# Optimization experiments

Measured on AMD Instinct MI355X. Metric: run time of the kernel, lower is better.

The kernel has to match this reference:

```python
import jax, jax.numpy as jnp
import numpy as np

B, T, V, E, H, FC, O = 4096, 64, 512, 32, 128, 256, 1024


def setup_inputs() -> dict:
    key = jax.random.key(0)
    ks = jax.random.split(key, 12)
    n = lambda k, shape, sc=1.0: (jax.random.normal(k, shape, jnp.float32) * sc)
    return {
        "message": n(ks[0], (B, T, V), 0.1),
        "W_emb": n(ks[1], (E, V), 0.05),
        "b_emb": n(ks[2], (E,), 0.05),
        "init_emb": n(ks[3], (1, 1, E), 1.0),
        "W_ih": n(ks[4], (3 * H, E), 0.08),
        "W_hh": n(ks[5], (3 * H, H), 0.08),
        "b_ih": n(ks[6], (3 * H,), 0.05),
        "b_hh": n(ks[7], (3 * H,), 0.05),
        "W_fc1": n(ks[8], (FC, H), 0.08),
        "b_fc1": n(ks[9], (FC,), 0.05),
        "W_fc2": n(ks[10], (O, FC), 0.05),
        "b_fc2": n(ks[11], (O,), 0.05),
    }


def reference(message, W_emb, b_emb, init_emb, W_ih, W_hh, b_ih, b_hh,
              W_fc1, b_fc1, W_fc2, b_fc2):
    Bb, Tt, Vv = message.shape
    Hh = W_hh.shape[1]
    # Per-step embedding of the message (torch does this inside the loop;
    # it is a pure per-timestep linear so we batch it once): [B,T,E]
    emb = jnp.einsum('btv,ev->bte', message, W_emb) + b_emb
    # Inputs consumed by the GRU at step t: initial_embedding at t=0,
    # then embedding(message[:, t-1]) for t >= 1. The embedding of the
    # final token is computed in torch but never fed to the GRU.
    x0 = jnp.broadcast_to(init_emb[0], (Bb, init_emb.shape[-1]))  # [B,E]
    xs = jnp.concatenate([x0[:, None, :], emb[:, :Tt - 1, :]], axis=1)  # [B,T,E]
    # Precompute input-side gate pre-activations for all steps: [T,B,3H]
    gi_all = jnp.einsum('bte,ge->tbg', xs, W_ih) + b_ih

    def gru_step(h, gi):
        gh = h @ W_hh.T + b_hh  # [B,3H]
        i_r, i_z, i_n = jnp.split(gi, 3, axis=-1)
        h_r, h_z, h_n = jnp.split(gh, 3, axis=-1)
        r = jax.nn.sigmoid(i_r + h_r)
        z = jax.nn.sigmoid(i_z + h_z)
        nng = jnp.tanh(i_n + r * h_n)
        h_new = (1.0 - z) * nng + z * h
        return h_new, None

    h0 = jnp.zeros((Bb, Hh), message.dtype)
    h_last, _ = jax.lax.scan(gru_step, h0, gi_all)
    hid = jax.nn.elu(h_last @ W_fc1.T + b_fc1)
    return jax.nn.sigmoid(hid @ W_fc2.T + b_fc2)
```

## Files before the change

### kernel.cpp

```cpp
#include <hip/hip_runtime.h>
#include <math.h>

#define B_ 4096
#define T_ 64
#define V_ 512
#define E_ 32
#define H_ 128
#define FC1_ 256
#define O_ 1024

typedef float f32x4 __attribute__((ext_vector_type(4)));
typedef short s16x8 __attribute__((ext_vector_type(8)));
typedef unsigned short u16;

#define MFMA16(a, b, c) __builtin_amdgcn_mfma_f32_16x16x32_bf16(a, b, c, 0, 0, 0)

union Frag { u16 q[8]; unsigned u[4]; s16x8 v; };

__device__ __forceinline__ u16 f2bf(float f) {
    union { float f; unsigned u; } v; v.f = f;
    unsigned r = v.u + 0x7FFFu + ((v.u >> 16) & 1u);
    return (u16)(r >> 16);
}
__device__ __forceinline__ unsigned cvtpk(float lo, float hi) {
    unsigned r;
    asm("v_cvt_pk_bf16_f32 %0, %1, %2" : "=v"(r) : "v"(lo), "v"(hi));
    return r;
}
__device__ __forceinline__ float sigf(float x) { return 1.0f / (1.0f + __expf(-x)); }
__device__ __forceinline__ float tanhfast(float x) {
    return 1.0f - 2.0f / (__expf(2.0f * x) + 1.0f);
}
__device__ __forceinline__ void gll16(const float* gsrc, float* ldst) {
    __builtin_amdgcn_global_load_lds(
        (const __attribute__((address_space(1))) unsigned int*)gsrc,
        (__attribute__((address_space(3))) unsigned int*)ldst,
        16, 0, 0);
}
__device__ __forceinline__ s16x8 gatherB(const float* W, int row, int K, int k0, int lh) {
    const float* p = W + (size_t)row * K + k0 + lh * 8;
    float4 a = *(const float4*)p;
    float4 b = *(const float4*)(p + 4);
    Frag f;
    f.u[0] = cvtpk(a.x, a.y); f.u[1] = cvtpk(a.z, a.w);
    f.u[2] = cvtpk(b.x, b.y); f.u[3] = cvtpk(b.z, b.w);
    return f.v;
}

__global__ void __launch_bounds__(512, 2) fused_kernel(
    const float* __restrict__ msg,
    const float* __restrict__ Wemb, const float* __restrict__ b_emb,
    const float* __restrict__ init_emb,
    const float* __restrict__ Wih, const float* __restrict__ Whh,
    const float* __restrict__ b_ih, const float* __restrict__ b_hh,
    const float* __restrict__ Wfc1, const float* __restrict__ b_fc1,
    const float* __restrict__ Wfc2, const float* __restrict__ b_fc2,
    float* __restrict__ out) {
    __shared__ float mlds[2][16][516];
    __shared__ u16 hlds[2][16 * 136];
    __shared__ float epart[2][8][576];
    __shared__ u16 xfrag[2][640];
    __shared__ u16 hidl[16 * 264];
    const int tid = threadIdx.x, w = tid >> 6, l = tid & 63;
    const int ln = l & 15, lh = l >> 4;
    const int wg = w & 3, wp = w >> 2;
    const int gb = blockIdx.x;

    for (int i = tid; i < 16 * 136; i += 512) hlds[0][i] = 0;

#define GLL_COL(C, BUF) do {                                                   \
    _Pragma("unroll")                                                          \
    for (int i_ = 0; i_ < 4; i_++) {                                           \
        int r_ = 2 * w + (i_ >> 1);                                            \
        int h_ = (i_ & 1) * 256;                                               \
        gll16(msg + ((size_t)(gb * 16 + r_) * T_ + (C)) * V_ + h_ + l * 4,     \
              &mlds[BUF][r_][h_]);                                             \
    }                                                                          \
} while (0)

    GLL_COL(0, 0);
    GLL_COL(1, 1);

    s16x8 wh[3][4], wi[3], we[2][2];
    float br, bz, bin, bgn;
    {
        #pragma unroll
        for (int g = 0; g < 3; g++) {
            int gt = wg + 4 * wp + 8 * g;
            #pragma unroll
            for (int kc = 0; kc < 4; kc++)
                wh[g][kc] = gatherB(Whh, gt * 16 + ln, 128, kc * 32, lh);
            wi[g] = gatherB(Wih, gt * 16 + ln, 32, 0, lh);
        }
        #pragma unroll
        for (int kk = 0; kk < 2; kk++) {
            we[kk][0] = gatherB(Wemb, ln, 512, (2 * w + kk) * 32, lh);
            we[kk][1] = gatherB(Wemb, 16 + ln, 512, (2 * w + kk) * 32, lh);
        }
        int c = wg * 16 + wp * 64 + ln;
        br  = b_ih[c] + b_hh[c];
        bz  = b_ih[128 + c] + b_hh[128 + c];
        bin = b_ih[256 + c];
        bgn = b_hh[256 + c];
    }
    const float bev = b_emb[tid & 31];
    s16x8 xinit;
    {
        Frag xi;
        #pragma unroll
        for (int j = 0; j < 8; j++) xi.q[j] = f2bf(init_emb[lh * 8 + j]);
        xinit = xi.v;
    }
    float hold[4] = {};
    __syncthreads();

#define EMBED_LDS(BUF, PAR) do {                                               \
    f32x4 e0 = {0.f, 0.f, 0.f, 0.f}, e1 = {0.f, 0.f, 0.f, 0.f};                \
    _Pragma("unroll")                                                          \
    for (int kk = 0; kk < 2; kk++) {                                           \
        const float* mp = &mlds[BUF][ln][(2 * w + kk) * 32 + lh * 8];          \
        f32x4 m0 = *(const f32x4*)mp;                                          \
        f32x4 m1 = *(const f32x4*)(mp + 4);                                    \
        Frag fa;                                                               \
        fa.u[0] = cvtpk(m0[0], m0[1]); fa.u[1] = cvtpk(m0[2], m0[3]);          \
        fa.u[2] = cvtpk(m1[0], m1[1]); fa.u[3] = cvtpk(m1[2], m1[3]);          \
        e0 = MFMA16(fa.v, we[kk][0], e0);                                      \
        e1 = MFMA16(fa.v, we[kk][1], e1);                                      \
    }                                                                          \
    _Pragma("unroll")                                                          \
    for (int i = 0; i < 4; i++) {                                              \
        epart[PAR][w][(lh * 4 + i) * 36 + ln]      = e0[i];                    \
        epart[PAR][w][(lh * 4 + i) * 36 + 16 + ln] = e1[i];                    \
    }                                                                          \
} while (0)

    EMBED_LDS(0, 1);
    __syncthreads();

    const int aoff = ln * 136 + lh * 8;
    const int colo = wg * 16 + wp * 64 + ln;
    const int fr = tid >> 5, fc = tid & 31, fo = fr * 36 + fc;

#define GRU_STEP(TT) do {                                                      \
    const int t = (TT);                                                        \
    if (t <= 60) GLL_COL(t + 2, t & 1);                                        \
    const u16* hb = hlds[t & 1];                                               \
    s16x8 af0 = *(const s16x8*)(hb + aoff);                                    \
    s16x8 af1 = *(const s16x8*)(hb + aoff + 32);                               \
    s16x8 af2 = *(const s16x8*)(hb + aoff + 64);                               \
    s16x8 af3 = *(const s16x8*)(hb + aoff + 96);                               \
    s16x8 xc;                                                                  \
    if (t == 0) xc = xinit;                                                    \
    else xc = *(const s16x8*)(&xfrag[(t + 1) & 1][0] + ln * 40 + lh * 8);      \
    f32x4 ar  = {br, br, br, br};                                              \
    f32x4 az  = {bz, bz, bz, bz};                                              \
    f32x4 agn = {bgn, bgn, bgn, bgn};                                          \
    f32x4 ain = {bin, bin, bin, bin};                                          \
    ar  = MFMA16(xc, wi[0], ar);                                               \
    az  = MFMA16(xc, wi[1], az);                                               \
    ain = MFMA16(xc, wi[2], ain);                                              \
    ar  = MFMA16(af0, wh[0][0], ar);                                           \
    ar  = MFMA16(af1, wh[0][1], ar);                                           \
    ar  = MFMA16(af2, wh[0][2], ar);                                           \
    ar  = MFMA16(af3, wh[0][3], ar);                                           \
    az  = MFMA16(af0, wh[1][0], az);                                           \
    az  = MFMA16(af1, wh[1][1], az);                                           \
    az  = MFMA16(af2, wh[1][2], az);                                           \
    az  = MFMA16(af3, wh[1][3], az);                                           \
    agn = MFMA16(af0, wh[2][0], agn);                                          \
    agn = MFMA16(af1, wh[2][1], agn);                                          \
    agn = MFMA16(af2, wh[2][2], agn);                                          \
    agn = MFMA16(af3, wh[2][3], agn);                                          \
    u16* hw = hlds[(t + 1) & 1];                                               \
    float hn[4];                                                               \
    _Pragma("unroll")                                                          \
    for (int i = 0; i < 4; i++) {                                              \
        float rg = sigf(ar[i]);                                                \
        float zg = sigf(az[i]);                                                \
        float ng = tanhfast(ain[i] + rg * agn[i]);                             \
        hn[i] = zg * (hold[i] - ng) + ng;                                      \
        hold[i] = hn[i];                                                       \
    }                                                                          \
    {                                                                          \
        unsigned u01 = cvtpk(hn[0], hn[1]);                                    \
        unsigned u23 = cvtpk(hn[2], hn[3]);                                    \
        hw[(lh * 4 + 0) * 136 + colo] = (u16)(u01 & 0xFFFFu);                  \
        hw[(lh * 4 + 1) * 136 + colo] = (u16)(u01 >> 16);                      \
        hw[(lh * 4 + 2) * 136 + colo] = (u16)(u23 & 0xFFFFu);                  \
        hw[(lh * 4 + 3) * 136 + colo] = (u16)(u23 >> 16);                      \
    }                                                                          \
    if (t <= 61) EMBED_LDS((t + 1) & 1, t & 1);                                \
    if (t <= 62) {                                                             \
        const float* eb = &epart[(t + 1) & 1][0][0];                           \
        float s = eb[fo]           + eb[576 + fo]     + eb[2 * 576 + fo]       \
                + eb[3 * 576 + fo] + eb[4 * 576 + fo] + eb[5 * 576 + fo]       \
                + eb[6 * 576 + fo] + eb[7 * 576 + fo] + bev;                   \
        xfrag[t & 1][fr * 40 + fc] = f2bf(s);                                  \
    }                                                                          \
    __syncthreads();                                                           \
} while (0)

    for (int tt = 0; tt < 64; tt += 2) {
        GRU_STEP(tt);
        GRU_STEP(tt + 1);
    }
#undef GRU_STEP
#undef GLL_COL
#undef EMBED_LDS

    const u16* hb = hlds[0];
    s16x8 hf0 = *(const s16x8*)(hb + aoff);
    s16x8 hf1 = *(const s16x8*)(hb + aoff + 32);
    s16x8 hf2 = *(const s16x8*)(hb + aoff + 64);
    s16x8 hf3 = *(const s16x8*)(hb + aoff + 96);
    #pragma unroll
    for (int q = 0; q < 2; q++) {
        int ot = 2 * w + q;
        float b1 = b_fc1[ot * 16 + ln];
        f32x4 a1 = {b1, b1, b1, b1};
        a1 = MFMA16(hf0, gatherB(Wfc1, ot * 16 + ln, 128, 0,  lh), a1);
        a1 = MFMA16(hf1, gatherB(Wfc1, ot * 16 + ln, 128, 32, lh), a1);
        a1 = MFMA16(hf2, gatherB(Wfc1, ot * 16 + ln, 128, 64, lh), a1);
        a1 = MFMA16(hf3, gatherB(Wfc1, ot * 16 + ln, 128, 96, lh), a1);
        #pragma unroll
        for (int i = 0; i < 4; i++) {
            float v = a1[i];
            v = v > 0.0f ? v : (__expf(v) - 1.0f);
            hidl[(lh * 4 + i) * 264 + ot * 16 + ln] = f2bf(v);
        }
    }
    __syncthreads();

    s16x8 hf[8];
    #pragma unroll
    for (int kc = 0; kc < 8; kc++)
        hf[kc] = *(const s16x8*)(hidl + ln * 264 + kc * 32 + lh * 8);
    #pragma unroll
    for (int q = 0; q < 8; q++) {
        int nt = 8 * w + q;
        float b2 = b_fc2[nt * 16 + ln];
        f32x4 a2 = {b2, b2, b2, b2};
        #pragma unroll
        for (int kc = 0; kc < 8; kc++)
            a2 = MFMA16(hf[kc], gatherB(Wfc2, nt * 16 + ln, 256, kc * 32, lh), a2);
        #pragma unroll
        for (int i = 0; i < 4; i++)
            out[(size_t)(gb * 16 + lh * 4 + i) * 1024 + nt * 16 + ln] = sigf(a2[i]);
    }
}

extern "C" void kernel_launch(void* const* d_in, const int* in_sizes, int n_in,
                              void* d_out, int out_size, void* d_ws, size_t ws_size,
                              hipStream_t stream) {
    const float* message  = (const float*)d_in[0];
    const float* W_emb    = (const float*)d_in[1];
    const float* b_emb    = (const float*)d_in[2];
    const float* init_emb = (const float*)d_in[3];
    const float* W_ih     = (const float*)d_in[4];
    const float* W_hh     = (const float*)d_in[5];
    const float* b_ih     = (const float*)d_in[6];
    const float* b_hh     = (const float*)d_in[7];
    const float* W_fc1    = (const float*)d_in[8];
    const float* b_fc1    = (const float*)d_in[9];
    const float* W_fc2    = (const float*)d_in[10];
    const float* b_fc2    = (const float*)d_in[11];
    float* out = (float*)d_out;
    (void)d_ws; (void)ws_size;

    hipLaunchKernelGGL(fused_kernel, dim3(256), dim3(512), 0, stream,
                       message, W_emb, b_emb, init_emb, W_ih, W_hh, b_ih, b_hh,
                       W_fc1, b_fc1, W_fc2, b_fc2, out);
}
```

Baseline: 158.1 us.

## Triple-buffer message prefetch with partial vmcnt barriers in GRU loop

Moves the message-column prefetch to three LDS buffers so loads are issued three steps ahead, and replaces __syncthreads with an explicit barrier that waits only until at most 4 global loads remain outstanding. This lets each wave keep one step's async global-to-LDS copies in flight across the barrier instead of draining them every step. The initial embedding is now written into xfrag up front so the t==0 branch disappears, and the loop is unrolled by 6 with compile-time buffer indices. The hidl buffer is aliased onto epart to offset the added LDS, which could still affect occupancy, and the hand-tuned vmcnt count must match the loads actually issued.

```diff
diff --git a/kernel.cpp b/kernel.cpp
--- a/kernel.cpp
+++ b/kernel.cpp
@@ -46,6 +46,16 @@
     f.u[2] = cvtpk(b.x, b.y); f.u[3] = cvtpk(b.z, b.w);
     return f.v;
 }
+
+#define STEP_BARRIER() do {                                        \
+    asm volatile("s_waitcnt vmcnt(4) lgkmcnt(0)" ::: "memory");    \
+    __builtin_amdgcn_s_barrier();                                  \
+    __builtin_amdgcn_sched_barrier(0);                             \
+} while (0)
+#define LDS_BARRIER() do {                                         \
+    asm volatile("s_waitcnt lgkmcnt(0)" ::: "memory");             \
+    __builtin_amdgcn_s_barrier();                                  \
+} while (0)
 
 __global__ void __launch_bounds__(512, 2) fused_kernel(
     const float* __restrict__ msg,
@@ -56,17 +66,21 @@
     const float* __restrict__ Wfc1, const float* __restrict__ b_fc1,
     const float* __restrict__ Wfc2, const float* __restrict__ b_fc2,
     float* __restrict__ out) {
-    __shared__ float mlds[2][16][516];
+    __shared__ float mlds[3][16][516];
     __shared__ u16 hlds[2][16 * 136];
     __shared__ float epart[2][8][576];
     __shared__ u16 xfrag[2][640];
-    __shared__ u16 hidl[16 * 264];
+    u16* const hidl = (u16*)&epart[0][0][0];
     const int tid = threadIdx.x, w = tid >> 6, l = tid & 63;
     const int ln = l & 15, lh = l >> 4;
     const int wg = w & 3, wp = w >> 2;
     const int gb = blockIdx.x;
 
     for (int i = tid; i < 16 * 136; i += 512) hlds[0][i] = 0;
+    {
+        int fr = tid >> 5, fc = tid & 31;
+        xfrag[1][fr * 40 + fc] = f2bf(init_emb[fc]);
+    }
 
 #define GLL_COL(C, BUF) do {                                                   \
     _Pragma("unroll")                                                          \
@@ -80,6 +94,7 @@
 
     GLL_COL(0, 0);
     GLL_COL(1, 1);
+    GLL_COL(2, 2);
 
     s16x8 wh[3][4], wi[3], we[2][2];
     float br, bz, bin, bgn;
@@ -104,13 +119,6 @@
         bgn = b_hh[256 + c];
     }
     const float bev = b_emb[tid & 31];
-    s16x8 xinit;
-    {
-        Frag xi;
-        #pragma unroll
-        for (int j = 0; j < 8; j++) xi.q[j] = f2bf(init_emb[lh * 8 + j]);
-        xinit = xi.v;
-    }
     float hold[4] = {};
     __syncthreads();
 
@@ -135,23 +143,21 @@
 } while (0)
 
     EMBED_LDS(0, 1);
-    __syncthreads();
+    LDS_BARRIER();
 
     const int aoff = ln * 136 + lh * 8;
     const int colo = wg * 16 + wp * 64 + ln;
     const int fr = tid >> 5, fc = tid & 31, fo = fr * 36 + fc;
 
-#define GRU_STEP(TT) do {                                                      \
+#define GRU_STEP(TT, K, ISSUE, EMB, RED) do {                                  \
     const int t = (TT);                                                        \
-    if (t <= 60) GLL_COL(t + 2, t & 1);                                        \
-    const u16* hb = hlds[t & 1];                                               \
+    if (ISSUE) GLL_COL(t + 3, (K) % 3);                                        \
+    const u16* hb = hlds[(K) & 1];                                             \
     s16x8 af0 = *(const s16x8*)(hb + aoff);                                    \
     s16x8 af1 = *(const s16x8*)(hb + aoff + 32);                               \
     s16x8 af2 = *(const s16x8*)(hb + aoff + 64);                               \
     s16x8 af3 = *(const s16x8*)(hb + aoff + 96);                               \
-    s16x8 xc;                                                                  \
-    if (t == 0) xc = xinit;                                                    \
-    else xc = *(const s16x8*)(&xfrag[(t + 1) & 1][0] + ln * 40 + lh * 8);      \
+    s16x8 xc = *(const s16x8*)(&xfrag[((K) + 1) & 1][0] + ln * 40 + lh * 8);   \
     f32x4 ar  = {br, br, br, br};                                              \
     f32x4 az  = {bz, bz, bz, bz};                                              \
     f32x4 agn = {bgn, bgn, bgn, bgn};                                          \
@@ -171,7 +177,7 @@
     agn = MFMA16(af1, wh[2][1], agn);                                          \
     agn = MFMA16(af2, wh[2][2], agn);                                          \
     agn = MFMA16(af3, wh[2][3], agn);                                          \
-    u16* hw = hlds[(t + 1) & 1];                                               \
+    u16* hw = hlds[((K) + 1) & 1];                                             \
     float hn[4];                                                               \
     _Pragma("unroll")                                                          \
     for (int i = 0; i < 4; i++) {                                              \
@@ -189,21 +195,29 @@
         hw[(lh * 4 + 2) * 136 + colo] = (u16)(u23 & 0xFFFFu);                  \
         hw[(lh * 4 + 3) * 136 + colo] = (u16)(u23 >> 16);                      \
     }                                                                          \
-    if (t <= 61) EMBED_LDS((t + 1) & 1, t & 1);                                \
-    if (t <= 62) {                                                             \
-        const float* eb = &epart[(t + 1) & 1][0][0];                           \
+    if (EMB) EMBED_LDS(((K) + 1) % 3, (K) & 1);                                \
+    if (RED) {                                                                 \
+        const float* eb = &epart[((K) + 1) & 1][0][0];                         \
         float s = eb[fo]           + eb[576 + fo]     + eb[2 * 576 + fo]       \
                 + eb[3 * 576 + fo] + eb[4 * 576 + fo] + eb[5 * 576 + fo]       \
                 + eb[6 * 576 + fo] + eb[7 * 576 + fo] + bev;                   \
-        xfrag[t & 1][fr * 40 + fc] = f2bf(s);                                  \
-    }                                                                          \
-    __syncthreads();                                                           \
-} while (0)
-
-    for (int tt = 0; tt < 64; tt += 2) {
-        GRU_STEP(tt);
-        GRU_STEP(tt + 1);
-    }
+        xfrag[(K) & 1][fr * 40 + fc] = f2bf(s);                                \
+    }                                                                          \
+    STEP_BARRIER();                                                            \
+} while (0)
+
+    for (int tt = 0; tt < 60; tt += 6) {
+        GRU_STEP(tt + 0, 0, 1, 1, 1);
+        GRU_STEP(tt + 1, 1, 1, 1, 1);
+        GRU_STEP(tt + 2, 2, 1, 1, 1);
+        GRU_STEP(tt + 3, 3, 1, 1, 1);
+        GRU_STEP(tt + 4, 4, 1, 1, 1);
+        GRU_STEP(tt + 5, 5, 1, 1, 1);
+    }
+    GRU_STEP(60, 0, 1, 1, 1);
+    GRU_STEP(61, 1, 0, 1, 1);
+    GRU_STEP(62, 2, 0, 0, 1);
+    GRU_STEP(63, 3, 0, 0, 0);
 #undef GRU_STEP
 #undef GLL_COL
 #undef EMBED_LDS
@@ -229,7 +243,7 @@
             hidl[(lh * 4 + i) * 264 + ot * 16 + ln] = f2bf(v);
         }
     }
-    __syncthreads();
+    LDS_BARRIER();
 
     s16x8 hf[8];
     #pragma unroll
```

New measurement: 163.2 us. 3.2% more time.
